# Kernel optimization log

Measured on AMD Instinct MI355X. Metric: run time of the kernel, lower is better.

Reference implementation:

```python
import jax, jax.numpy as jnp
import numpy as np

S_LOCAL = 3
N_HEADS = 8
EPS = 1e-6


def setup_inputs() -> dict:
    key = jax.random.key(0)
    ks = jax.random.split(key, 9)
    B, D, T, H, W = 2, 512, 96, 16, 16
    std = 0.02
    return {
        "x": jax.random.normal(ks[0], (B, D, T, H, W), dtype=jnp.float32),
        "ln_gamma": jnp.ones((D,), dtype=jnp.float32),
        "ln_beta": jnp.zeros((D,), dtype=jnp.float32),
        "Wq": jax.random.normal(ks[1], (D, D), dtype=jnp.float32) * std,
        "Wk": jax.random.normal(ks[2], (D, D), dtype=jnp.float32) * std,
        "Wv": jax.random.normal(ks[3], (D, D), dtype=jnp.float32) * std,
        "Wkl": jax.random.normal(ks[4], (D, D), dtype=jnp.float32) * std,
        "Wvl": jax.random.normal(ks[5], (D, D), dtype=jnp.float32) * std,
        "Wo": jax.random.normal(ks[6], (D, D), dtype=jnp.float32) * std,
        "q_bias": jax.random.normal(ks[7], (1, N_HEADS, 1, D // N_HEADS), dtype=jnp.float32) * std,
    }


def _unfold_windows(x, s):
    # x: [..., T] -> [..., T, s] sliding windows with zero padding s//2 each side
    p = s // 2
    xp = jnp.pad(x, [(0, 0)] * (x.ndim - 1) + [(p, p)])
    T = x.shape[-1]
    idx = jnp.arange(T)[:, None] + jnp.arange(s)[None, :]  # [T, s]
    return xp[..., idx]


def reference(x, ln_gamma, ln_beta, Wq, Wk, Wv, Wkl, Wvl, Wo, q_bias):
    B, D, T, H, W = x.shape
    nh, dh, s = N_HEADS, D // N_HEADS, S_LOCAL
    factor = dh ** (-0.5)
    N = B * H * W

    # [B,D,T,H,W] -> [N, T, D]
    xt = jnp.transpose(x, (0, 3, 4, 2, 1)).reshape(N, T, D)

    # LayerNorm over D
    mu = xt.mean(-1, keepdims=True)
    var = xt.var(-1, keepdims=True)
    xn = (xt - mu) / jnp.sqrt(var + EPS) * ln_gamma + ln_beta

    # projections -> [N, nh, T, dh]
    def heads(y):
        return jnp.transpose(y.reshape(N, T, nh, dh), (0, 2, 1, 3))

    q = heads(xn @ Wq.T) + q_bias
    k = heads(xn @ Wk.T)
    v = heads(xn @ Wv.T)

    # global attention scores [N, nh, T, T]
    attn_global = jnp.einsum('bhnd,bhgd->bhng', q, k) * factor

    # local k/v: [N, T, D] -> [N, D, T] -> windows [N, D, T, s]
    kl = jnp.transpose(xn @ Wkl.T, (0, 2, 1))
    vl = jnp.transpose(xn @ Wvl.T, (0, 2, 1))
    k_w = jnp.transpose(_unfold_windows(kl, s).reshape(N, nh, dh, T, s), (0, 1, 3, 2, 4))  # [N,nh,T,dh,s]
    v_w = jnp.transpose(_unfold_windows(vl, s).reshape(N, nh, dh, T, s), (0, 1, 3, 2, 4))

    # local mask: True where window element came from zero padding -> [T, s]
    mask_local = _unfold_windows(jnp.ones((T,), dtype=jnp.float32), s) == 0

    attn_local = jnp.einsum('bhnd,bhndl->bhnl', q, k_w)
    attn_local = jnp.where(mask_local, -jnp.inf, attn_local) * factor

    # joint softmax over [T global + s local]
    attn_map = jax.nn.softmax(jnp.concatenate([attn_global, attn_local], axis=-1), axis=-1)
    ag, al = attn_map[..., :T], attn_map[..., T:]

    x_global = jnp.einsum('bhng,bhgd->bhnd', ag, v)
    x_local = jnp.einsum('bhnl,bhndl->bhnd', al, v_w)

    out = (jnp.transpose(x_global + x_local, (0, 2, 1, 3)).reshape(N, T, D)) @ Wo.T
    return jnp.transpose(out.reshape(B, H, W, T, D), (0, 4, 3, 1, 2))
```

## Files before the change

kernel.cpp:

```cpp
#include <hip/hip_runtime.h>
#include <hip/hip_fp16.h>
#include <cstdint>
#include <cstddef>

typedef _Float16 f16;
typedef _Float16 half8 __attribute__((ext_vector_type(8)));
typedef _Float16 half4v __attribute__((ext_vector_type(4)));
typedef float floatx4 __attribute__((ext_vector_type(4)));

#define MTOT 49152

__device__ __forceinline__ void gload_lds16(const f16* g, f16* l) {
  __builtin_amdgcn_global_load_lds((const __attribute__((address_space(1))) void*)g,
                                   (__attribute__((address_space(3))) void*)l, 16, 0, 0);
}

__device__ __forceinline__ half8 load_h8u(const f16* p) {
  half8 v;
  __builtin_memcpy(&v, p, 16);
  return v;
}

__global__ __launch_bounds__(256) void wconv_kernel(
    const float* __restrict__ Wq, const float* __restrict__ Wk,
    const float* __restrict__ Wv, const float* __restrict__ Wkl,
    const float* __restrict__ Wvl, const float* __restrict__ Wo,
    f16* __restrict__ WQKV, f16* __restrict__ WO) {
  int idx = blockIdx.x * 256 + threadIdx.x;
  if (idx < 2560 * 512) {
    int row = idx >> 9;
    int col = idx & 511;
    int seg = row >> 9;
    int r = row & 511;
    const float* src;
    switch (seg) {
      case 0: src = Wq; break;
      case 1: src = Wk; break;
      case 2: src = Wkl; break;
      case 3: src = Wvl; break;
      default: src = Wv; break;
    }
    WQKV[idx] = (f16)src[r * 512 + col];
  }
  if (idx < 512 * 512) WO[idx] = (f16)Wo[idx];
}

__global__ __launch_bounds__(256) void ln_kernel(
    const float* __restrict__ x, const float* __restrict__ gamma,
    const float* __restrict__ beta, f16* __restrict__ XN) {
  const int hwg = blockIdx.x & 3;
  const int t   = (blockIdx.x >> 2) % 96;
  const int b   = blockIdx.x / (4 * 96);
  const int lhw = threadIdx.x & 63;
  const int dg  = threadIdx.x >> 6;
  const int hw  = hwg * 64 + lhw;
  const float* xp = x + (size_t)b * 512 * 24576 + (size_t)t * 256 + hw;

  float s = 0.f, s2 = 0.f;
  for (int d = dg * 128; d < dg * 128 + 128; ++d) {
    float v = xp[(size_t)d * 24576];
    s += v;
    s2 += v * v;
  }
  __shared__ float S1[4][64], S2[4][64];
  S1[dg][lhw] = s;
  S2[dg][lhw] = s2;
  __syncthreads();
  s  = S1[0][lhw] + S1[1][lhw] + S1[2][lhw] + S1[3][lhw];
  s2 = S2[0][lhw] + S2[1][lhw] + S2[2][lhw] + S2[3][lhw];
  const float mean = s * (1.f / 512.f);
  float var = s2 * (1.f / 512.f) - mean * mean;
  var = fmaxf(var, 0.f);
  const float rstd = rsqrtf(var + 1e-6f);
  const int n = b * 256 + hw;
  f16* outp = XN + ((size_t)n * 96 + t) * 512;
  for (int d0 = dg * 128; d0 < dg * 128 + 128; d0 += 8) {
    half8 buf;
#pragma unroll
    for (int j = 0; j < 8; ++j) {
      float v = xp[(size_t)(d0 + j) * 24576];
      buf[j] = (f16)((v - mean) * rstd * gamma[d0 + j] + beta[d0 + j]);
    }
    *(half8*)(outp + d0) = buf;
  }
}

__global__ __launch_bounds__(512, 2) void gemmA_kernel(
    const f16* __restrict__ A, const f16* __restrict__ B,
    f16* __restrict__ Cqkv, const float* __restrict__ qbias) {
  __shared__ f16 LA[2][256 * 64];
  __shared__ f16 LB[2][256 * 64];
  __shared__ __align__(16) f16 esc[8][16][72];

  const int lin = blockIdx.x;
  const int cpx = (int)gridDim.x >> 3;
  const int swz = (lin & 7) * cpx + (lin >> 3);
  const int o = ((gridDim.x & 7) == 0) ? swz : lin;
  const int mt = o / 10;
  const int nt = o % 10;
  const int m0 = mt * 256;
  const int n0 = nt * 256;

  const int tid = threadIdx.x;
  const int wid = tid >> 6;
  const int lane = tid & 63;
  const int wm = wid >> 2;
  const int wn = wid & 3;
  const int l15 = lane & 15, l4 = lane >> 4;

  const int srow = tid >> 3;
  const int scol = ((tid & 7) ^ (srow & 7)) * 8;
  const f16* Abase = A + (size_t)(m0 + srow) * 512 + scol;
  const f16* Bbase = B + (size_t)(n0 + srow) * 512 + scol;

  const int cks0 = ((l4) ^ (l15 & 7)) * 8;
  const int cks1 = ((4 + l4) ^ (l15 & 7)) * 8;
  const int arow = wm * 128 + l15;
  const int brow = wn * 64 + l15;

  floatx4 acc[8][4] = {};
  half8 a_f[4][2];
  half8 b_f[4][2];

  auto stageH = [&](int slot, int kt, int mat, int h) {
    const f16* g = (mat ? Bbase : Abase) + kt * 64 + (size_t)(h * 128) * 512;
    f16* l = (mat ? LB[slot] : LA[slot]) + h * 8192 + tid * 8;
    gload_lds16(g, l);
    gload_lds16(g + (size_t)64 * 512, l + 4096);
  };

  stageH(0, 0, 0, 0); stageH(0, 0, 0, 1);
  stageH(0, 0, 1, 0); stageH(0, 0, 1, 1);
  stageH(1, 1, 0, 0); stageH(1, 1, 0, 1);
  asm volatile("s_waitcnt vmcnt(4)" ::: "memory");
  __builtin_amdgcn_s_barrier();

#pragma unroll
  for (int kt = 0; kt < 8; ++kt) {
    const f16* As = LA[kt & 1];
    const f16* Bs = LB[kt & 1];
    const int nsl = (kt + 1) & 1;

#pragma unroll
    for (int mf2 = 0; mf2 < 4; ++mf2) {
      a_f[mf2][0] = *(const half8*)(As + (arow + mf2 * 16) * 64 + cks0);
      a_f[mf2][1] = *(const half8*)(As + (arow + mf2 * 16) * 64 + cks1);
    }
#pragma unroll
    for (int nf = 0; nf < 2; ++nf) {
      b_f[nf][0] = *(const half8*)(Bs + (brow + nf * 16) * 64 + cks0);
      b_f[nf][1] = *(const half8*)(Bs + (brow + nf * 16) * 64 + cks1);
    }
    if (kt + 1 < 8) { stageH(nsl, kt + 1, 1, 0); stageH(nsl, kt + 1, 1, 1); }
    __builtin_amdgcn_s_barrier();
    __builtin_amdgcn_s_setprio(1);
#pragma unroll
    for (int mf2 = 0; mf2 < 4; ++mf2)
#pragma unroll
      for (int nf2 = 0; nf2 < 2; ++nf2)
#pragma unroll
        for (int ks = 0; ks < 2; ++ks)
          acc[mf2][nf2] = __builtin_amdgcn_mfma_f32_16x16x32_f16(
              a_f[mf2][ks], b_f[nf2][ks], acc[mf2][nf2], 0, 0, 0);
    __builtin_amdgcn_s_setprio(0);
    __builtin_amdgcn_s_barrier();

#pragma unroll
    for (int nf = 2; nf < 4; ++nf) {
      b_f[nf][0] = *(const half8*)(Bs + (brow + nf * 16) * 64 + cks0);
      b_f[nf][1] = *(const half8*)(Bs + (brow + nf * 16) * 64 + cks1);
    }
    __builtin_amdgcn_s_barrier();
    __builtin_amdgcn_s_setprio(1);
#pragma unroll
    for (int mf2 = 0; mf2 < 4; ++mf2)
#pragma unroll
      for (int nf2 = 0; nf2 < 2; ++nf2)
#pragma unroll
        for (int ks = 0; ks < 2; ++ks)
          acc[mf2][2 + nf2] = __builtin_amdgcn_mfma_f32_16x16x32_f16(
              a_f[mf2][ks], b_f[2 + nf2][ks], acc[mf2][2 + nf2], 0, 0, 0);
    __builtin_amdgcn_s_setprio(0);
    __builtin_amdgcn_s_barrier();

#pragma unroll
    for (int mf2 = 0; mf2 < 4; ++mf2) {
      a_f[mf2][0] = *(const half8*)(As + (arow + 64 + mf2 * 16) * 64 + cks0);
      a_f[mf2][1] = *(const half8*)(As + (arow + 64 + mf2 * 16) * 64 + cks1);
    }
    __builtin_amdgcn_s_barrier();
    __builtin_amdgcn_s_setprio(1);
#pragma unroll
    for (int mf2 = 0; mf2 < 4; ++mf2)
#pragma unroll
      for (int nf2 = 0; nf2 < 2; ++nf2)
#pragma unroll
        for (int ks = 0; ks < 2; ++ks)
          acc[4 + mf2][nf2] = __builtin_amdgcn_mfma_f32_16x16x32_f16(
              a_f[mf2][ks], b_f[nf2][ks], acc[4 + mf2][nf2], 0, 0, 0);
    __builtin_amdgcn_s_setprio(0);
    __builtin_amdgcn_s_barrier();

    if (kt + 2 < 8) { stageH(kt & 1, kt + 2, 0, 0); stageH(kt & 1, kt + 2, 0, 1); }
    __builtin_amdgcn_s_barrier();
    __builtin_amdgcn_s_setprio(1);
#pragma unroll
    for (int mf2 = 0; mf2 < 4; ++mf2)
#pragma unroll
      for (int nf2 = 0; nf2 < 2; ++nf2)
#pragma unroll
        for (int ks = 0; ks < 2; ++ks)
          acc[4 + mf2][2 + nf2] = __builtin_amdgcn_mfma_f32_16x16x32_f16(
              a_f[mf2][ks], b_f[2 + nf2][ks], acc[4 + mf2][2 + nf2], 0, 0, 0);
    __builtin_amdgcn_s_setprio(0);
    if (kt < 6) {
      asm volatile("s_waitcnt vmcnt(4)" ::: "memory");
    } else if (kt == 6) {
      asm volatile("s_waitcnt vmcnt(0)" ::: "memory");
    }
    __builtin_amdgcn_s_barrier();
  }

  float bias[4], scl[4];
#pragma unroll
  for (int nf = 0; nf < 4; ++nf) {
    const int n = n0 + wn * 64 + nf * 16 + l15;
    const bool isq = (n < 512);
    bias[nf] = isq ? qbias[n] : 0.0f;
    scl[nf]  = isq ? 0.125f : 1.0f;
  }
  const int rrow = lane >> 2;
  const int rcg  = lane & 3;
#pragma unroll
  for (int mf = 0; mf < 8; ++mf) {
#pragma unroll
    for (int nf = 0; nf < 4; ++nf)
#pragma unroll
      for (int j = 0; j < 4; ++j)
        esc[wid][l4 * 4 + j][nf * 16 + l15] = (f16)((acc[mf][nf][j] + bias[nf]) * scl[nf]);
    asm volatile("s_waitcnt lgkmcnt(0)" ::: "memory");
    half8 v0 = *(const half8*)(&esc[wid][rrow][rcg * 16]);
    half8 v1 = *(const half8*)(&esc[wid][rrow][rcg * 16 + 8]);
    asm volatile("" ::: "memory");
    f16* dst = Cqkv + (size_t)(m0 + wm * 128 + mf * 16 + rrow) * 2560 + n0 + wn * 64 + rcg * 16;
    *(half8*)dst = v0;
    *(half8*)(dst + 8) = v1;
  }
}

__global__ __launch_bounds__(256) void gemmO_kernel(
    const f16* __restrict__ A, const f16* __restrict__ B,
    float* __restrict__ Out) {
  __shared__ f16 As[2][128 * 32];
  __shared__ f16 Bs[2][128 * 32];

  const int lin = blockIdx.x;
  const int cpx = (int)gridDim.x >> 3;
  const int o = (lin & 7) * cpx + (lin >> 3);
  const int nt = o >> 2;
  const int mt = o & 3;
  const int m0 = mt * 128;
  const int n0 = nt * 128;
  const int tid = threadIdx.x;
  const int lane = tid & 63;
  const int wid = tid >> 6;
  const int wm = wid >> 1, wn = wid & 1;
  const int l15 = lane & 15, l4 = lane >> 4;

  floatx4 acc[4][4] = {};

  const int srow = tid >> 2;
  const int skp = (((tid & 3) ^ ((tid >> 3) & 3))) * 8;
  const f16* ap = A + (size_t)(m0 + srow) * 512 + skp;
  const f16* bp = B + (size_t)(n0 + srow) * 512 + skp;

  auto stage = [&](int buf, int k0) {
    f16* asl = As[buf] + tid * 8;
    f16* bsl = Bs[buf] + tid * 8;
    gload_lds16(ap + k0, asl);
    gload_lds16(ap + (size_t)64 * 512 + k0, asl + 2048);
    gload_lds16(bp + k0, bsl);
    gload_lds16(bp + (size_t)64 * 512 + k0, bsl + 2048);
  };

  const int rc = (l4 ^ ((l15 >> 1) & 3)) * 8;

  stage(0, 0);
  __syncthreads();
  int cur = 0;
  for (int k0 = 0; k0 < 512; k0 += 32) {
    if (k0 + 32 < 512) stage(cur ^ 1, k0 + 32);
    half8 af[4], bf[4];
#pragma unroll
    for (int mf = 0; mf < 4; ++mf)
      af[mf] = *(const half8*)(As[cur] + (wm * 64 + mf * 16 + l15) * 32 + rc);
#pragma unroll
    for (int nf = 0; nf < 4; ++nf)
      bf[nf] = *(const half8*)(Bs[cur] + (wn * 64 + nf * 16 + l15) * 32 + rc);
#pragma unroll
    for (int mf = 0; mf < 4; ++mf)
#pragma unroll
      for (int nf = 0; nf < 4; ++nf)
        acc[mf][nf] = __builtin_amdgcn_mfma_f32_16x16x32_f16(af[mf], bf[nf], acc[mf][nf], 0, 0, 0);
    __syncthreads();
    cur ^= 1;
  }

  const int mbase = m0 + wm * 64;
  const int nbase = n0 + wn * 64;
#pragma unroll
  for (int nf = 0; nf < 4; ++nf) {
    const int m2 = nbase + nf * 16 + l15;
    const int bb = m2 / 24576;
    const int rem = m2 - bb * 24576;
    const int t = rem >> 8;
    const int hw = rem & 255;
    float* op = Out + ((size_t)bb * 512 * 96 + t) * 256 + hw;
#pragma unroll
    for (int mf = 0; mf < 4; ++mf) {
#pragma unroll
      for (int j = 0; j < 4; ++j) {
        const int d = mbase + mf * 16 + l4 * 4 + j;
        __builtin_nontemporal_store(acc[mf][nf][j], op + (size_t)d * 24576);
      }
    }
  }
}

__global__ __launch_bounds__(192) void attn_kernel(
    const f16* __restrict__ QKV, f16* __restrict__ AO, int n0chunk) {
  const int nn = blockIdx.x >> 3;
  const int h = blockIdx.x & 7;
  const int tid = threadIdx.x;
  const int wid = tid >> 6;
  const int lane = tid & 63;
  const int l15 = lane & 15, l4 = lane >> 4;
  const int nglob = n0chunk + nn;
  const int bb = nglob >> 8, hw = nglob & 255;

  __shared__ __align__(16) f16 VTl[64][112];
  __shared__ __align__(16) f16 VLTl[64][112];
  __shared__ __align__(16) float locS[3][16][4];
  __shared__ __align__(16) f16 pS[3][16][104];
  __shared__ __align__(16) f16 pS2[3][16][40];
  __shared__ __align__(16) f16 oesc[3][16][72];

  const f16* base = QKV + (size_t)nn * 96 * 2560;

#pragma unroll
  for (int it = 0; it < 4; ++it) {
    const int r = (tid >> 3) + it * 24;
    const int c0 = (tid & 7) * 8;
    half8 v  = *(const half8*)(base + (size_t)r * 2560 + 2048 + h * 64 + c0);
    half8 vl = *(const half8*)(base + (size_t)r * 2560 + 1536 + h * 64 + c0);
#pragma unroll
    for (int j = 0; j < 8; ++j) {
      VTl[c0 + j][r]  = v[j];
      VLTl[c0 + j][r] = vl[j];
    }
  }
  if (tid < 128) {
    half8 z = {};
    *(half8*)(&VLTl[tid >> 1][96 + (tid & 1) * 8]) = z;
  }

  half8 kb[6][2];
#pragma unroll
  for (int nf = 0; nf < 6; ++nf)
#pragma unroll
    for (int kg = 0; kg < 2; ++kg)
      kb[nf][kg] = *(const half8*)(base + (size_t)(nf * 16 + l15) * 2560 + 512 + h * 64 + kg * 32 + l4 * 8);

  __syncthreads();

  for (int mb = wid * 2; mb < wid * 2 + 2; ++mb) {
    const int t0 = mb * 16;
    const int tb = (t0 >= 2) ? (t0 - 2) : 0;
    const int d0 = t0 - 1 - tb;

    half8 aq[2], kl1[2], kl2[2];
    {
      int r1 = t0 - 1 + l15; if (r1 < 0) r1 = 0;
      int r2 = t0 + 1 + l15; if (r2 > 95) r2 = 95;
#pragma unroll
      for (int kg = 0; kg < 2; ++kg) {
        aq[kg]  = *(const half8*)(base + (size_t)(t0 + l15) * 2560 + h * 64 + kg * 32 + l4 * 8);
        kl1[kg] = *(const half8*)(base + (size_t)r1 * 2560 + 1024 + h * 64 + kg * 32 + l4 * 8);
        kl2[kg] = *(const half8*)(base + (size_t)r2 * 2560 + 1024 + h * 64 + kg * 32 + l4 * 8);
      }
    }

    floatx4 s[6] = {};
    floatx4 sl1 = {}, sl2 = {};
#pragma unroll
    for (int nf = 0; nf < 6; ++nf)
#pragma unroll
      for (int kg = 0; kg < 2; ++kg)
        s[nf] = __builtin_amdgcn_mfma_f32_16x16x32_f16(aq[kg], kb[nf][kg], s[nf], 0, 0, 0);
#pragma unroll
    for (int kg = 0; kg < 2; ++kg) {
      sl1 = __builtin_amdgcn_mfma_f32_16x16x32_f16(aq[kg], kl1[kg], sl1, 0, 0, 0);
      sl2 = __builtin_amdgcn_mfma_f32_16x16x32_f16(aq[kg], kl2[kg], sl2, 0, 0, 0);
    }

    half8 vb[4][3], vlb[4];
#pragma unroll
    for (int nf = 0; nf < 4; ++nf) {
#pragma unroll
      for (int kg = 0; kg < 3; ++kg)
        vb[nf][kg] = *(const half8*)(&VTl[nf * 16 + l15][kg * 32 + l4 * 8]);
      vlb[nf] = load_h8u(&VLTl[nf * 16 + l15][tb + l4 * 8]);
    }

    {
      half8 z = {};
      f16* pz = &pS2[wid][0][0];
      *(half8*)(pz + lane * 8) = z;
      if (lane < 16) *(half8*)(pz + 512 + lane * 8) = z;
    }
#pragma unroll
    for (int j = 0; j < 4; ++j) {
      const int r = l4 * 4 + j;
      const int s1i = l15 - r;
      if (s1i >= 0 && s1i < 3) locS[wid][r][s1i] = sl1[j];
      const int s2i = l15 + 2 - r;
      if (l15 >= 14 && s2i >= 0 && s2i < 3) locS[wid][r][s2i] = sl2[j];
    }
    __syncthreads();

#pragma unroll
    for (int j = 0; j < 4; ++j) {
      const int row = l4 * 4 + j;
      float sv[6];
#pragma unroll
      for (int nf = 0; nf < 6; ++nf) sv[nf] = s[nf][j];
      float mx = sv[0];
#pragma unroll
      for (int nf = 1; nf < 6; ++nf) mx = fmaxf(mx, sv[nf]);
      for (int off = 1; off < 16; off <<= 1) mx = fmaxf(mx, __shfl_xor(mx, off, 64));
      const float l0 = (t0 + row >= 1)  ? locS[wid][row][0] : -__builtin_inff();
      const float l1 = locS[wid][row][1];
      const float l2 = (t0 + row <= 94) ? locS[wid][row][2] : -__builtin_inff();
      mx = fmaxf(mx, fmaxf(l0, fmaxf(l1, l2)));
      float e[6], sum = 0.f;
#pragma unroll
      for (int nf = 0; nf < 6; ++nf) {
        e[nf] = expf(sv[nf] - mx);
        sum += e[nf];
      }
      for (int off = 1; off < 16; off <<= 1) sum += __shfl_xor(sum, off, 64);
      const float e0 = expf(l0 - mx), e1 = expf(l1 - mx), e2 = expf(l2 - mx);
      sum += e0 + e1 + e2;
      const float rd = 1.0f / sum;
#pragma unroll
      for (int nf = 0; nf < 6; ++nf) pS[wid][row][nf * 16 + l15] = (f16)(e[nf] * rd);
      if (l15 < 3) {
        const int w = row + l15 + d0;
        const float ev = (l15 == 0) ? e0 : ((l15 == 1) ? e1 : e2);
        if (w >= 0) pS2[wid][row][w] = (f16)(ev * rd);
      }
    }
    __syncthreads();

    floatx4 o[4] = {};
    half8 pfr[3];
#pragma unroll
    for (int kg = 0; kg < 3; ++kg)
      pfr[kg] = *(const half8*)(&pS[wid][l15][kg * 32 + l4 * 8]);
    half8 pf2 = *(const half8*)(&pS2[wid][l15][l4 * 8]);
#pragma unroll
    for (int nf = 0; nf < 4; ++nf) {
#pragma unroll
      for (int kg = 0; kg < 3; ++kg)
        o[nf] = __builtin_amdgcn_mfma_f32_16x16x32_f16(pfr[kg], vb[nf][kg], o[nf], 0, 0, 0);
      o[nf] = __builtin_amdgcn_mfma_f32_16x16x32_f16(pf2, vlb[nf], o[nf], 0, 0, 0);
    }

#pragma unroll
    for (int nf = 0; nf < 4; ++nf)
#pragma unroll
      for (int j = 0; j < 4; ++j)
        oesc[wid][l4 * 4 + j][nf * 16 + l15] = (f16)o[nf][j];
    asm volatile("s_waitcnt lgkmcnt(0)" ::: "memory");
    {
      const int rrow = lane >> 2;
      const int rcg  = lane & 3;
      half8 v0 = *(const half8*)(&oesc[wid][rrow][rcg * 16]);
      half8 v1 = *(const half8*)(&oesc[wid][rrow][rcg * 16 + 8]);
      asm volatile("" ::: "memory");
      f16* dst = AO + ((size_t)(bb * 96 + t0 + rrow) * 256 + hw) * 512 + h * 64 + rcg * 16;
      *(half8*)dst = v0;
      *(half8*)(dst + 8) = v1;
    }
  }
}

extern "C" void kernel_launch(void* const* d_in, const int* in_sizes, int n_in,
                              void* d_out, int out_size, void* d_ws, size_t ws_size,
                              hipStream_t stream) {
  (void)in_sizes; (void)n_in; (void)out_size;
  const float* x     = (const float*)d_in[0];
  const float* gamma = (const float*)d_in[1];
  const float* beta  = (const float*)d_in[2];
  const float* Wq    = (const float*)d_in[3];
  const float* Wk    = (const float*)d_in[4];
  const float* Wv    = (const float*)d_in[5];
  const float* Wkl   = (const float*)d_in[6];
  const float* Wvl   = (const float*)d_in[7];
  const float* Wo    = (const float*)d_in[8];
  const float* qb    = (const float*)d_in[9];
  float* out = (float*)d_out;

  char* ws = (char*)d_ws;
  size_t off = 0;
  auto alloc = [&](size_t bytes) -> void* {
    void* p = ws + off;
    off += (bytes + 255) & ~(size_t)255;
    return p;
  };
  f16* XN   = (f16*)alloc((size_t)MTOT * 512 * 2);
  f16* AO   = (f16*)alloc((size_t)MTOT * 512 * 2);
  f16* WQKV = (f16*)alloc((size_t)2560 * 512 * 2);
  f16* WOh  = (f16*)alloc((size_t)512 * 512 * 2);
  int cn = 512;
  while (cn > 32 && off + (size_t)cn * 96 * 2560 * 2 + 256 > ws_size)
    cn >>= 1;
  f16* QKVc = (f16*)alloc((size_t)cn * 96 * 2560 * 2);

  wconv_kernel<<<5120, 256, 0, stream>>>(Wq, Wk, Wv, Wkl, Wvl, Wo, WQKV, WOh);
  ln_kernel<<<768, 256, 0, stream>>>(x, gamma, beta, XN);

  const int nch = 512 / cn;
  for (int c = 0; c < nch; ++c) {
    const int mtiles = (cn * 96) / 256;
    gemmA_kernel<<<mtiles * 10, 512, 0, stream>>>(XN + (size_t)c * cn * 96 * 512,
                                                  WQKV, QKVc, qb);
    attn_kernel<<<cn * 8, 192, 0, stream>>>(QKVc, AO, c * cn);
  }
  gemmO_kernel<<<1536, 256, 0, stream>>>(WOh, AO, out);
}
```

Before: 426.2 us.

## Make QKV GEMM persistent with cross-tile prefetch of next tile operands

The QKV projection GEMM now launches a fixed grid of 240 blocks, and each block loops over several consecutive 256x256 output tiles. The next tile's first K-slices are prefetched during the current tile's final iterations, and the staging is reorganised into finer half-tile loads spread across the four MFMA phases. The aim is to hide per-tile prologue latency and tail effects. The catch is that tiles/240 must divide exactly; otherwise tiles are silently dropped, which is why the minimum chunk size was raised to 64.

New measurement: 441.0 us. 3.5% more time.

```diff
diff --git a/kernel.cpp b/kernel.cpp
--- a/kernel.cpp
+++ b/kernel.cpp
@@ -87,19 +87,14 @@
 
 __global__ __launch_bounds__(512, 2) void gemmA_kernel(
     const f16* __restrict__ A, const f16* __restrict__ B,
-    f16* __restrict__ Cqkv, const float* __restrict__ qbias) {
+    f16* __restrict__ Cqkv, const float* __restrict__ qbias, int tpb) {
   __shared__ f16 LA[2][256 * 64];
   __shared__ f16 LB[2][256 * 64];
   __shared__ __align__(16) f16 esc[8][16][72];
 
-  const int lin = blockIdx.x;
   const int cpx = (int)gridDim.x >> 3;
-  const int swz = (lin & 7) * cpx + (lin >> 3);
-  const int o = ((gridDim.x & 7) == 0) ? swz : lin;
-  const int mt = o / 10;
-  const int nt = o % 10;
-  const int m0 = mt * 256;
-  const int n0 = nt * 256;
+  const int b = ((int)blockIdx.x & 7) * cpx + ((int)blockIdx.x >> 3);
+  const int g0 = b * tpb;
 
   const int tid = threadIdx.x;
   const int wid = tid >> 6;
@@ -110,141 +105,172 @@
 
   const int srow = tid >> 3;
   const int scol = ((tid & 7) ^ (srow & 7)) * 8;
-  const f16* Abase = A + (size_t)(m0 + srow) * 512 + scol;
-  const f16* Bbase = B + (size_t)(n0 + srow) * 512 + scol;
 
   const int cks0 = ((l4) ^ (l15 & 7)) * 8;
   const int cks1 = ((4 + l4) ^ (l15 & 7)) * 8;
   const int arow = wm * 128 + l15;
   const int brow = wn * 64 + l15;
 
-  floatx4 acc[8][4] = {};
-  half8 a_f[4][2];
-  half8 b_f[4][2];
-
-  auto stageH = [&](int slot, int kt, int mat, int h) {
-    const f16* g = (mat ? Bbase : Abase) + kt * 64 + (size_t)(h * 128) * 512;
-    f16* l = (mat ? LB[slot] : LA[slot]) + h * 8192 + tid * 8;
+  auto tileBase = [&](int g, const f16*& Ab, const f16*& Bb) {
+    const int mt = g / 10, nt = g % 10;
+    Ab = A + (size_t)(mt * 256 + srow) * 512 + scol;
+    Bb = B + (size_t)(nt * 256 + srow) * 512 + scol;
+  };
+
+  auto stageH = [&](int slot, int kt, const f16* gb, int isB, int h) {
+    const f16* g = gb + kt * 64 + (size_t)(h * 128) * 512;
+    f16* l = (isB ? LB[slot] : LA[slot]) + h * 8192 + tid * 8;
     gload_lds16(g, l);
     gload_lds16(g + (size_t)64 * 512, l + 4096);
   };
 
-  stageH(0, 0, 0, 0); stageH(0, 0, 0, 1);
-  stageH(0, 0, 1, 0); stageH(0, 0, 1, 1);
-  stageH(1, 1, 0, 0); stageH(1, 1, 0, 1);
-  asm volatile("s_waitcnt vmcnt(4)" ::: "memory");
+  const f16 *Ab, *Bb;
+  const f16 *An = nullptr, *Bn = nullptr;
+  tileBase(g0, Ab, Bb);
+
+  stageH(0, 0, Ab, 0, 0); stageH(0, 0, Ab, 0, 1);
+  stageH(0, 0, Bb, 1, 0); stageH(0, 0, Bb, 1, 1);
+  stageH(1, 1, Ab, 0, 0);
+  asm volatile("s_waitcnt vmcnt(2)" ::: "memory");
   __builtin_amdgcn_s_barrier();
 
-#pragma unroll
-  for (int kt = 0; kt < 8; ++kt) {
-    const f16* As = LA[kt & 1];
-    const f16* Bs = LB[kt & 1];
-    const int nsl = (kt + 1) & 1;
-
-#pragma unroll
-    for (int mf2 = 0; mf2 < 4; ++mf2) {
-      a_f[mf2][0] = *(const half8*)(As + (arow + mf2 * 16) * 64 + cks0);
-      a_f[mf2][1] = *(const half8*)(As + (arow + mf2 * 16) * 64 + cks1);
-    }
-#pragma unroll
-    for (int nf = 0; nf < 2; ++nf) {
-      b_f[nf][0] = *(const half8*)(Bs + (brow + nf * 16) * 64 + cks0);
-      b_f[nf][1] = *(const half8*)(Bs + (brow + nf * 16) * 64 + cks1);
-    }
-    if (kt + 1 < 8) { stageH(nsl, kt + 1, 1, 0); stageH(nsl, kt + 1, 1, 1); }
-    __builtin_amdgcn_s_barrier();
-    __builtin_amdgcn_s_setprio(1);
-#pragma unroll
-    for (int mf2 = 0; mf2 < 4; ++mf2)
-#pragma unroll
-      for (int nf2 = 0; nf2 < 2; ++nf2)
-#pragma unroll
-        for (int ks = 0; ks < 2; ++ks)
-          acc[mf2][nf2] = __builtin_amdgcn_mfma_f32_16x16x32_f16(
-              a_f[mf2][ks], b_f[nf2][ks], acc[mf2][nf2], 0, 0, 0);
-    __builtin_amdgcn_s_setprio(0);
-    __builtin_amdgcn_s_barrier();
-
-#pragma unroll
-    for (int nf = 2; nf < 4; ++nf) {
-      b_f[nf][0] = *(const half8*)(Bs + (brow + nf * 16) * 64 + cks0);
-      b_f[nf][1] = *(const half8*)(Bs + (brow + nf * 16) * 64 + cks1);
-    }
-    __builtin_amdgcn_s_barrier();
-    __builtin_amdgcn_s_setprio(1);
-#pragma unroll
-    for (int mf2 = 0; mf2 < 4; ++mf2)
-#pragma unroll
-      for (int nf2 = 0; nf2 < 2; ++nf2)
-#pragma unroll
-        for (int ks = 0; ks < 2; ++ks)
-          acc[mf2][2 + nf2] = __builtin_amdgcn_mfma_f32_16x16x32_f16(
-              a_f[mf2][ks], b_f[2 + nf2][ks], acc[mf2][2 + nf2], 0, 0, 0);
-    __builtin_amdgcn_s_setprio(0);
-    __builtin_amdgcn_s_barrier();
-
-#pragma unroll
-    for (int mf2 = 0; mf2 < 4; ++mf2) {
-      a_f[mf2][0] = *(const half8*)(As + (arow + 64 + mf2 * 16) * 64 + cks0);
-      a_f[mf2][1] = *(const half8*)(As + (arow + 64 + mf2 * 16) * 64 + cks1);
-    }
-    __builtin_amdgcn_s_barrier();
-    __builtin_amdgcn_s_setprio(1);
-#pragma unroll
-    for (int mf2 = 0; mf2 < 4; ++mf2)
-#pragma unroll
-      for (int nf2 = 0; nf2 < 2; ++nf2)
-#pragma unroll
-        for (int ks = 0; ks < 2; ++ks)
-          acc[4 + mf2][nf2] = __builtin_amdgcn_mfma_f32_16x16x32_f16(
-              a_f[mf2][ks], b_f[nf2][ks], acc[4 + mf2][nf2], 0, 0, 0);
-    __builtin_amdgcn_s_setprio(0);
-    __builtin_amdgcn_s_barrier();
-
-    if (kt + 2 < 8) { stageH(kt & 1, kt + 2, 0, 0); stageH(kt & 1, kt + 2, 0, 1); }
-    __builtin_amdgcn_s_barrier();
-    __builtin_amdgcn_s_setprio(1);
-#pragma unroll
-    for (int mf2 = 0; mf2 < 4; ++mf2)
-#pragma unroll
-      for (int nf2 = 0; nf2 < 2; ++nf2)
-#pragma unroll
-        for (int ks = 0; ks < 2; ++ks)
-          acc[4 + mf2][2 + nf2] = __builtin_amdgcn_mfma_f32_16x16x32_f16(
-              a_f[mf2][ks], b_f[2 + nf2][ks], acc[4 + mf2][2 + nf2], 0, 0, 0);
-    __builtin_amdgcn_s_setprio(0);
-    if (kt < 6) {
-      asm volatile("s_waitcnt vmcnt(4)" ::: "memory");
-    } else if (kt == 6) {
-      asm volatile("s_waitcnt vmcnt(0)" ::: "memory");
-    }
-    __builtin_amdgcn_s_barrier();
-  }
-
-  float bias[4], scl[4];
-#pragma unroll
-  for (int nf = 0; nf < 4; ++nf) {
-    const int n = n0 + wn * 64 + nf * 16 + l15;
-    const bool isq = (n < 512);
-    bias[nf] = isq ? qbias[n] : 0.0f;
-    scl[nf]  = isq ? 0.125f : 1.0f;
-  }
-  const int rrow = lane >> 2;
-  const int rcg  = lane & 3;
-#pragma unroll
-  for (int mf = 0; mf < 8; ++mf) {
-#pragma unroll
-    for (int nf = 0; nf < 4; ++nf)
-#pragma unroll
-      for (int j = 0; j < 4; ++j)
-        esc[wid][l4 * 4 + j][nf * 16 + l15] = (f16)((acc[mf][nf][j] + bias[nf]) * scl[nf]);
-    asm volatile("s_waitcnt lgkmcnt(0)" ::: "memory");
-    half8 v0 = *(const half8*)(&esc[wid][rrow][rcg * 16]);
-    half8 v1 = *(const half8*)(&esc[wid][rrow][rcg * 16 + 8]);
-    asm volatile("" ::: "memory");
-    f16* dst = Cqkv + (size_t)(m0 + wm * 128 + mf * 16 + rrow) * 2560 + n0 + wn * 64 + rcg * 16;
-    *(half8*)dst = v0;
-    *(half8*)(dst + 8) = v1;
+  for (int i = 0; i < tpb; ++i) {
+    const int g = g0 + i;
+    const int m0 = (g / 10) * 256;
+    const int n0 = (g % 10) * 256;
+    const bool lastt = (i + 1 == tpb);
+    if (!lastt) tileBase(g + 1, An, Bn);
+
+    floatx4 acc[8][4] = {};
+    half8 a_f[4][2];
+    half8 b_f[4][2];
+
+#pragma unroll
+    for (int kt = 0; kt < 8; ++kt) {
+      const f16* As = LA[kt & 1];
+      const f16* Bs = LB[kt & 1];
+      const int nsl = (kt + 1) & 1;
+
+#pragma unroll
+      for (int mf2 = 0; mf2 < 4; ++mf2) {
+        a_f[mf2][0] = *(const half8*)(As + (arow + mf2 * 16) * 64 + cks0);
+        a_f[mf2][1] = *(const half8*)(As + (arow + mf2 * 16) * 64 + cks1);
+      }
+#pragma unroll
+      for (int nf = 0; nf < 2; ++nf) {
+        b_f[nf][0] = *(const half8*)(Bs + (brow + nf * 16) * 64 + cks0);
+        b_f[nf][1] = *(const half8*)(Bs + (brow + nf * 16) * 64 + cks1);
+      }
+      if (kt < 7) stageH(nsl, kt + 1, Ab, 0, 1);
+      else if (!lastt) stageH(0, 0, An, 0, 1);
+      __builtin_amdgcn_s_barrier();
+      __builtin_amdgcn_s_setprio(1);
+#pragma unroll
+      for (int mf2 = 0; mf2 < 4; ++mf2)
+#pragma unroll
+        for (int nf2 = 0; nf2 < 2; ++nf2)
+#pragma unroll
+          for (int ks = 0; ks < 2; ++ks)
+            acc[mf2][nf2] = __builtin_amdgcn_mfma_f32_16x16x32_f16(
+                a_f[mf2][ks], b_f[nf2][ks], acc[mf2][nf2], 0, 0, 0);
+      __builtin_amdgcn_s_setprio(0);
+      __builtin_amdgcn_s_barrier();
+
+#pragma unroll
+      for (int nf = 2; nf < 4; ++nf) {
+        b_f[nf][0] = *(const half8*)(Bs + (brow + nf * 16) * 64 + cks0);
+        b_f[nf][1] = *(const half8*)(Bs + (brow + nf * 16) * 64 + cks1);
+      }
+      if (kt < 7) stageH(nsl, kt + 1, Bb, 1, 0);
+      else if (!lastt) stageH(0, 0, Bn, 1, 0);
+      __builtin_amdgcn_s_barrier();
+      __builtin_amdgcn_s_setprio(1);
+#pragma unroll
+      for (int mf2 = 0; mf2 < 4; ++mf2)
+#pragma unroll
+        for (int nf2 = 0; nf2 < 2; ++nf2)
+#pragma unroll
+          for (int ks = 0; ks < 2; ++ks)
+            acc[mf2][2 + nf2] = __builtin_amdgcn_mfma_f32_16x16x32_f16(
+                a_f[mf2][ks], b_f[2 + nf2][ks], acc[mf2][2 + nf2], 0, 0, 0);
+      __builtin_amdgcn_s_setprio(0);
+      __builtin_amdgcn_s_barrier();
+
+#pragma unroll
+      for (int mf2 = 0; mf2 < 4; ++mf2) {
+        a_f[mf2][0] = *(const half8*)(As + (arow + 64 + mf2 * 16) * 64 + cks0);
+        a_f[mf2][1] = *(const half8*)(As + (arow + 64 + mf2 * 16) * 64 + cks1);
+      }
+      if (kt < 7) stageH(nsl, kt + 1, Bb, 1, 1);
+      else if (!lastt) stageH(0, 0, Bn, 1, 1);
+      __builtin_amdgcn_s_barrier();
+      __builtin_amdgcn_s_setprio(1);
+#pragma unroll
+      for (int mf2 = 0; mf2 < 4; ++mf2)
+#pragma unroll
+        for (int nf2 = 0; nf2 < 2; ++nf2)
+#pragma unroll
+          for (int ks = 0; ks < 2; ++ks)
+            acc[4 + mf2][nf2] = __builtin_amdgcn_mfma_f32_16x16x32_f16(
+                a_f[mf2][ks], b_f[nf2][ks], acc[4 + mf2][nf2], 0, 0, 0);
+      __builtin_amdgcn_s_setprio(0);
+      __builtin_amdgcn_s_barrier();
+
+      if (kt < 6) stageH(kt & 1, kt + 2, Ab, 0, 0);
+      else if (kt == 6) { if (!lastt) stageH(0, 0, An, 0, 0); }
+      else { if (!lastt) stageH(1, 1, An, 0, 0); }
+      __builtin_amdgcn_s_barrier();
+      __builtin_amdgcn_s_setprio(1);
+#pragma unroll
+      for (int mf2 = 0; mf2 < 4; ++mf2)
+#pragma unroll
+        for (int nf2 = 0; nf2 < 2; ++nf2)
+#pragma unroll
+          for (int ks = 0; ks < 2; ++ks)
+            acc[4 + mf2][2 + nf2] = __builtin_amdgcn_mfma_f32_16x16x32_f16(
+                a_f[mf2][ks], b_f[2 + nf2][ks], acc[4 + mf2][2 + nf2], 0, 0, 0);
+      __builtin_amdgcn_s_setprio(0);
+      if (kt < 6) {
+        asm volatile("s_waitcnt vmcnt(2)" ::: "memory");
+      } else if (kt == 6) {
+        if (lastt) asm volatile("s_waitcnt vmcnt(0)" ::: "memory");
+        else       asm volatile("s_waitcnt vmcnt(2)" ::: "memory");
+      }
+      __builtin_amdgcn_s_barrier();
+    }
+
+    float bias[4], scl[4];
+#pragma unroll
+    for (int nf = 0; nf < 4; ++nf) {
+      const int n = n0 + wn * 64 + nf * 16 + l15;
+      const bool isq = (n < 512);
+      bias[nf] = isq ? qbias[n] : 0.0f;
+      scl[nf]  = isq ? 0.125f : 1.0f;
+    }
+    const int rrow = lane >> 2;
+    const int rcg  = lane & 3;
+#pragma unroll
+    for (int mf = 0; mf < 8; ++mf) {
+#pragma unroll
+      for (int nf = 0; nf < 4; ++nf)
+#pragma unroll
+        for (int j = 0; j < 4; ++j)
+          esc[wid][l4 * 4 + j][nf * 16 + l15] = (f16)((acc[mf][nf][j] + bias[nf]) * scl[nf]);
+      asm volatile("s_waitcnt lgkmcnt(0)" ::: "memory");
+      half8 v0 = *(const half8*)(&esc[wid][rrow][rcg * 16]);
+      half8 v1 = *(const half8*)(&esc[wid][rrow][rcg * 16 + 8]);
+      asm volatile("" ::: "memory");
+      f16* dst = Cqkv + (size_t)(m0 + wm * 128 + mf * 16 + rrow) * 2560 + n0 + wn * 64 + rcg * 16;
+      *(half8*)dst = v0;
+      *(half8*)(dst + 8) = v1;
+    }
+
+    if (!lastt) {
+      asm volatile("s_waitcnt vmcnt(2)" ::: "memory");
+      __builtin_amdgcn_s_barrier();
+      Ab = An;
+      Bb = Bn;
+    }
   }
 }
 
@@ -523,7 +549,7 @@
   f16* WQKV = (f16*)alloc((size_t)2560 * 512 * 2);
   f16* WOh  = (f16*)alloc((size_t)512 * 512 * 2);
   int cn = 512;
-  while (cn > 32 && off + (size_t)cn * 96 * 2560 * 2 + 256 > ws_size)
+  while (cn > 64 && off + (size_t)cn * 96 * 2560 * 2 + 256 > ws_size)
     cn >>= 1;
   f16* QKVc = (f16*)alloc((size_t)cn * 96 * 2560 * 2);
 
@@ -532,9 +558,10 @@
 
   const int nch = 512 / cn;
   for (int c = 0; c < nch; ++c) {
-    const int mtiles = (cn * 96) / 256;
-    gemmA_kernel<<<mtiles * 10, 512, 0, stream>>>(XN + (size_t)c * cn * 96 * 512,
-                                                  WQKV, QKVc, qb);
+    const int tiles = (cn * 96 / 256) * 10;
+    const int tpb = tiles / 240;
+    gemmA_kernel<<<240, 512, 0, stream>>>(XN + (size_t)c * cn * 96 * 512,
+                                          WQKV, QKVc, qb, tpb);
     attn_kernel<<<cn * 8, 192, 0, stream>>>(QKVc, AO, c * cn);
   }
   gemmO_kernel<<<1536, 256, 0, stream>>>(WOh, AO, out);
```
